# Performance work log

Measured on AMD Instinct MI355X. Metric: run time of the kernel, lower is better.

The kernel has to match this reference:

```python
import jax, jax.numpy as jnp
import numpy as np

N_NODES = 50000
N_EDGES = 400000
IN_CH = 256
HID = 64
OUT_CH = 64
HEADS = 4
N_NTYPES = 3
N_ETYPES = 4
EDGE_DIM = 32
NEG_SLOPE = 0.2
LN_EPS = 1e-5


def _glorot(key, shape, fan_in, fan_out):
    gain = float(np.sqrt(2.0))  # calculate_gain('relu')
    limit = gain * np.sqrt(6.0 / (fan_in + fan_out))
    return jax.random.uniform(key, shape, jnp.float32, -limit, limit)


def setup_inputs() -> dict:
    key = jax.random.key(0)
    ks = jax.random.split(key, 24)
    HC1 = HEADS * HID
    inp = {
        'x': jax.random.normal(ks[0], (N_NODES, IN_CH), jnp.float32),
        'edge_index': jax.random.randint(ks[1], (2, N_EDGES), 0, N_NODES, jnp.int32),
        'node_type': jax.random.randint(ks[2], (N_NODES,), 0, N_NTYPES, jnp.int32),
        'edge_type': jax.random.randint(ks[3], (N_EDGES,), 0, N_ETYPES, jnp.int32),
        'edge_attr': jax.random.normal(ks[4], (N_EDGES, EDGE_DIM), jnp.float32),
        # layer 1 (in -> hid, concat=True)
        'W_src1': _glorot(ks[5], (N_NTYPES, IN_CH, HC1), IN_CH, HC1),
        'W_dst1': _glorot(ks[6], (N_NTYPES, IN_CH, HC1), IN_CH, HC1),
        'att_src1': _glorot(ks[7], (N_ETYPES, HEADS, HID), HEADS, HID),
        'att_dst1': _glorot(ks[8], (N_ETYPES, HEADS, HID), HEADS, HID),
        'W_edge1': _glorot(ks[9], (N_ETYPES, EDGE_DIM, HC1), EDGE_DIM, HC1),
        'att_edge1': _glorot(ks[10], (N_ETYPES, HEADS, HID), HEADS, HID),
        'bias1': jnp.zeros((HC1,), jnp.float32),
        'ln_gamma1': jnp.ones((HC1,), jnp.float32),
        'ln_beta1': jnp.zeros((HC1,), jnp.float32),
        # layer 2 (heads*hid -> out, concat=False)
        'W_src2': _glorot(ks[11], (N_NTYPES, HC1, HEADS * OUT_CH), HC1, HEADS * OUT_CH),
        'W_dst2': _glorot(ks[12], (N_NTYPES, HC1, HEADS * OUT_CH), HC1, HEADS * OUT_CH),
        'att_src2': _glorot(ks[13], (N_ETYPES, HEADS, OUT_CH), HEADS, OUT_CH),
        'att_dst2': _glorot(ks[14], (N_ETYPES, HEADS, OUT_CH), HEADS, OUT_CH),
        'W_edge2': _glorot(ks[15], (N_ETYPES, EDGE_DIM, HEADS * OUT_CH), EDGE_DIM, HEADS * OUT_CH),
        'att_edge2': _glorot(ks[16], (N_ETYPES, HEADS, OUT_CH), HEADS, OUT_CH),
        'bias2': jnp.zeros((OUT_CH,), jnp.float32),
    }
    return inp


def _htgat_conv(x, src, dst, node_type, edge_type, edge_attr,
                W_src, W_dst, att_src, att_dst, W_edge, att_edge, bias, concat):
    N = x.shape[0]
    T_e, H, C = att_src.shape
    # type-specific linear transforms: compute all types, select by node_type
    xs = jnp.einsum('nd,tdo->nto', x, W_src)  # [N, T_n, H*C]
    x_src = jnp.take_along_axis(xs, node_type[:, None, None], axis=1)[:, 0].reshape(N, H, C)
    xd = jnp.einsum('nd,tdo->nto', x, W_dst)
    x_dst = jnp.take_along_axis(xd, node_type[:, None, None], axis=1)[:, 0].reshape(N, H, C)
    # per-(node, edge_type) attention scores, gathered per edge
    s_src = jnp.einsum('nhc,thc->nth', x_src, att_src)  # [N, T_e, H]
    s_dst = jnp.einsum('nhc,thc->nth', x_dst, att_dst)
    et = edge_type[:, None, None]
    alpha = (jnp.take_along_axis(s_src[src], et, axis=1)[:, 0]
             + jnp.take_along_axis(s_dst[dst], et, axis=1)[:, 0])  # [E, H]
    # temporal edge contribution: (edge_attr @ W_edge[t]) . att_edge[t]
    v = jnp.einsum('tdhc,thc->tdh', W_edge.reshape(T_e, -1, H, C), att_edge)
    s_edge = jnp.einsum('ed,tdh->eth', edge_attr, v)  # [E, T_e, H]
    alpha = alpha + jnp.take_along_axis(s_edge, et, axis=1)[:, 0]
    alpha = jnp.where(alpha >= 0, alpha, NEG_SLOPE * alpha)  # leaky_relu
    # segment softmax over destination nodes
    amax = jax.ops.segment_max(alpha, dst, num_segments=N)  # [N, H]
    amax = jnp.where(jnp.isfinite(amax), amax, 0.0)
    ae = jnp.exp(alpha - amax[dst])
    denom = jax.ops.segment_sum(ae, dst, num_segments=N)
    attn = ae / (denom[dst] + 1e-16)  # [E, H]
    # weighted message aggregation (dropout is identity in eval mode)
    msg = x_src[src] * attn[:, :, None]  # [E, H, C]
    out = jax.ops.segment_sum(msg, dst, num_segments=N)  # [N, H, C]
    if concat:
        return out.reshape(N, H * C) + bias
    return out.mean(axis=1) + bias


def _layer_norm(x, gamma, beta):
    mu = x.mean(axis=-1, keepdims=True)
    var = ((x - mu) ** 2).mean(axis=-1, keepdims=True)
    return (x - mu) * jax.lax.rsqrt(var + LN_EPS) * gamma + beta


def reference(x, edge_index, node_type, edge_type, edge_attr,
              W_src1, W_dst1, att_src1, att_dst1, W_edge1, att_edge1, bias1,
              ln_gamma1, ln_beta1,
              W_src2, W_dst2, att_src2, att_dst2, W_edge2, att_edge2, bias2):
    src, dst = edge_index[0], edge_index[1]
    h = _htgat_conv(x, src, dst, node_type, edge_type, edge_attr,
                    W_src1, W_dst1, att_src1, att_dst1, W_edge1, att_edge1, bias1,
                    concat=True)
    h = _layer_norm(h, ln_gamma1, ln_beta1)
    h = jax.nn.elu(h)
    out = _htgat_conv(h, src, dst, node_type, edge_type, edge_attr,
                      W_src2, W_dst2, att_src2, att_dst2, W_edge2, att_edge2, bias2,
                      concat=False)
    return out
```

## Files before the change

kernel.cpp:

```cpp
#include <hip/hip_runtime.h>

#define NN 50000
#define NE 400000
#define NH 4
#define NTY 3
#define ETY 4
#define EDIM 32
#define NBLK 196
#define BM 32
#define GGRID ((NN + BM - 1) / BM + NTY)

typedef __attribute__((ext_vector_type(8))) short bf16x8;
typedef __attribute__((ext_vector_type(4))) float f32x4;

static __device__ __forceinline__ unsigned short f2bf(float f) {
    unsigned u = __float_as_uint(f);
    unsigned r = (u + 0x7FFFu + ((u >> 16) & 1u)) >> 16;
    return (unsigned short)r;
}
static __device__ __forceinline__ float bf2f(unsigned short s) {
    return __uint_as_float(((unsigned)s) << 16);
}

__global__ __launch_bounds__(256) void prep_fold(
    const float* __restrict__ W_dst1, const float* __restrict__ att_dst1,
    const float* __restrict__ W_edge1, const float* __restrict__ att_edge1,
    const float* __restrict__ W_dst2, const float* __restrict__ att_dst2,
    const float* __restrict__ W_edge2, const float* __restrict__ att_edge2,
    ushort* __restrict__ uf1, ushort* __restrict__ uf2,
    float* __restrict__ v1, float* __restrict__ v2)
{
    int idx = blockIdx.x * 256 + threadIdx.x;
    if (idx < 24576) {
        const float* W; const float* A; ushort* U; int i;
        if (idx < 12288) { W = W_dst1; A = att_dst1; U = uf1; i = idx; }
        else             { W = W_dst2; A = att_dst2; U = uf2; i = idx - 12288; }
        int d = i & 255, h = (i >> 8) & 3, t = (i >> 10) & 3, tn = i >> 12;
        const float* wp = W + tn * 65536 + d * 256 + h * 64;
        const float* ap = A + t * 256 + h * 64;
        float s = 0.f;
        #pragma unroll 8
        for (int c = 0; c < 64; ++c) s += wp[c] * ap[c];
        int th = t * 4 + h;
        int ks = d >> 5, g = (d >> 3) & 3, e = d & 7;
        U[(size_t)tn * 4096 + ks * 512 + (g * 16 + th) * 8 + e] = f2bf(s);
    } else {
        int i = idx - 24576;
        const float* W; const float* A; float* V;
        if (i < 512) { W = W_edge1; A = att_edge1; V = v1; }
        else         { W = W_edge2; A = att_edge2; V = v2; i -= 512; }
        int d = i & 31, h = (i >> 5) & 3, t = i >> 7;
        const float* wp = W + t * (EDIM * 256) + d * 256 + h * 64;
        const float* ap = A + t * 256 + h * 64;
        float s = 0.f;
        #pragma unroll 8
        for (int c = 0; c < 64; ++c) s += wp[c] * ap[c];
        V[(t * 4 + h) * 32 + d] = s;
    }
}

__global__ __launch_bounds__(256) void prep_wt(
    const float* __restrict__ W1, const float* __restrict__ W2,
    ushort* __restrict__ Wf1, ushort* __restrict__ Wf2)
{
    int idx = blockIdx.x * 256 + threadIdx.x;
    const int HALF = 196608;
    const float* W = (idx < HALF) ? W1 : W2;
    ushort* O = (idx < HALF) ? Wf1 : Wf2;
    int i = (idx < HALF) ? idx : idx - HALF;
    int n = i & 255, k = (i >> 8) & 255, t = i >> 16;
    int c16 = n >> 4, r16 = n & 15;
    int ks = k >> 5, g = (k >> 3) & 3, e = k & 7;
    O[(size_t)t * 65536 + (c16 * 8 + ks) * 512 + (g * 16 + r16) * 8 + e] =
        f2bf(W[(size_t)t * 65536 + k * 256 + n]);
}

__global__ void hist_k(const int* __restrict__ dst, int* __restrict__ cnt)
{
    int i = blockIdx.x * 256 + threadIdx.x;
    if (i < NE) atomicAdd(&cnt[dst[i]], 1);
}

__global__ __launch_bounds__(256) void csr_blocksum(
    const int* __restrict__ cnt, const int* __restrict__ ntype,
    int* __restrict__ blks)
{
    int tid = threadIdx.x, b = blockIdx.x;
    int j = b * 256 + tid;
    int c = (j < NN) ? cnt[j] : 0;
    int t = (j < NN) ? ntype[j] : 3;
    int p = (t < 3) ? (1 << (t * 10)) : 0;
    #pragma unroll
    for (int d = 1; d < 64; d <<= 1) { c += __shfl_xor(c, d); p += __shfl_xor(p, d); }
    __shared__ int ws[2][4];
    int lane = tid & 63, w = tid >> 6;
    if (lane == 0) { ws[0][w] = c; ws[1][w] = p; }
    __syncthreads();
    if (tid == 0) {
        int C = ws[0][0] + ws[0][1] + ws[0][2] + ws[0][3];
        int P = ws[1][0] + ws[1][1] + ws[1][2] + ws[1][3];
        blks[b]            = C;
        blks[NBLK + b]     = P & 1023;
        blks[2 * NBLK + b] = (P >> 10) & 1023;
        blks[3 * NBLK + b] = (P >> 20) & 1023;
    }
}

__global__ __launch_bounds__(256) void csr_scanmid(int* __restrict__ blks,
                                                   int* __restrict__ ntoff,
                                                   int* __restrict__ gblk)
{
    __shared__ int4 part[256];
    int tid = threadIdx.x;
    int4 v = make_int4(0, 0, 0, 0);
    if (tid < NBLK)
        v = make_int4(blks[tid], blks[NBLK + tid], blks[2 * NBLK + tid], blks[3 * NBLK + tid]);
    int4 orig = v;
    part[tid] = v;
    __syncthreads();
    for (int off = 1; off < 256; off <<= 1) {
        int4 u = (tid >= off) ? part[tid - off] : make_int4(0, 0, 0, 0);
        __syncthreads();
        part[tid].x += u.x; part[tid].y += u.y; part[tid].z += u.z; part[tid].w += u.w;
        __syncthreads();
    }
    int4 inc = part[tid];
    if (tid < NBLK) {
        blks[tid]            = inc.x - orig.x;
        blks[NBLK + tid]     = inc.y - orig.y;
        blks[2 * NBLK + tid] = inc.z - orig.z;
        blks[3 * NBLK + tid] = inc.w - orig.w;
    }
    if (tid == 255) {
        ntoff[0] = 0; ntoff[1] = inc.y; ntoff[2] = inc.y + inc.z;
        ntoff[3] = inc.y + inc.z + inc.w;
        int b0 = (inc.y + BM - 1) / BM;
        int b1 = (inc.z + BM - 1) / BM;
        int b2 = (inc.w + BM - 1) / BM;
        gblk[0] = 0; gblk[1] = b0; gblk[2] = b0 + b1; gblk[3] = b0 + b1 + b2;
    }
}

__global__ __launch_bounds__(256) void csr_apply(
    const int* __restrict__ cnt, const int* __restrict__ ntype,
    const int* __restrict__ blks, const int* __restrict__ ntoff,
    int* __restrict__ row_ptr, int* __restrict__ node_perm)
{
    int tid = threadIdx.x, b = blockIdx.x;
    int j = b * 256 + tid;
    int c = (j < NN) ? cnt[j] : 0;
    int t = (j < NN) ? ntype[j] : 3;
    int p = (t < 3) ? (1 << (t * 10)) : 0;
    int lane = tid & 63, w = tid >> 6;
    int ic = c, ip = p;
    #pragma unroll
    for (int d = 1; d < 64; d <<= 1) {
        int uc = __shfl_up(ic, d), up = __shfl_up(ip, d);
        if (lane >= d) { ic += uc; ip += up; }
    }
    __shared__ int ws[2][4];
    if (lane == 63) { ws[0][w] = ic; ws[1][w] = ip; }
    __syncthreads();
    int coff = 0, poff = 0;
    for (int i = 0; i < w; ++i) { coff += ws[0][i]; poff += ws[1][i]; }
    int exc  = ic - c + coff;
    int expp = ip - p + poff;
    if (j < NN) {
        row_ptr[j] = blks[b] + exc;
        if (t < 3) {
            int tb   = blks[(t + 1) * NBLK + b];
            int tpfx = (expp >> (t * 10)) & 1023;
            node_perm[ntoff[t] + tb + tpfx] = j;
        }
    }
    if (j == 0) row_ptr[NN] = NE;
}

__global__ void scatter_k(const int* __restrict__ src, const int* __restrict__ dst,
                          const int* __restrict__ etype,
                          const int* __restrict__ row_ptr, int* __restrict__ cursor,
                          int* __restrict__ spk, int* __restrict__ e2c)
{
    int i = blockIdx.x * 256 + threadIdx.x;
    if (i >= NE) return;
    int d = dst[i];
    int pos = row_ptr[d] + atomicAdd(&cursor[d], 1);
    spk[pos] = src[i] | (etype[i] << 16);
    e2c[i] = pos;
}

__global__ __launch_bounds__(256) void sedge_k(
    const float* __restrict__ eattr, const int* __restrict__ etype,
    const int* __restrict__ e2c,
    const float* __restrict__ v1, const float* __restrict__ v2,
    float* __restrict__ sedge1c, float* __restrict__ sedge2c)
{
    __shared__ float v1l[512], v2l[512];
    int tid = threadIdx.x;
    v1l[tid] = v1[tid]; v1l[tid + 256] = v1[tid + 256];
    v2l[tid] = v2[tid]; v2l[tid + 256] = v2[tid + 256];
    __syncthreads();

    int i = blockIdx.x * 256 + tid;
    if (i >= NE) return;
    int t = etype[i];
    int pos = e2c[i];
    float4 ea[8];
    #pragma unroll
    for (int q = 0; q < 8; ++q) ea[q] = *(const float4*)(eattr + (size_t)i * 32 + q * 4);
    float4 o1, o2;
    #pragma unroll
    for (int h = 0; h < 4; ++h) {
        const float* vp1 = v1l + (t * 4 + h) * 32;
        const float* vp2 = v2l + (t * 4 + h) * 32;
        float s1 = 0.f, s2 = 0.f;
        #pragma unroll
        for (int q = 0; q < 8; ++q) {
            float4 w1 = *(const float4*)(vp1 + q * 4);
            float4 w2 = *(const float4*)(vp2 + q * 4);
            s1 += ea[q].x * w1.x + ea[q].y * w1.y + ea[q].z * w1.z + ea[q].w * w1.w;
            s2 += ea[q].x * w2.x + ea[q].y * w2.y + ea[q].z * w2.z + ea[q].w * w2.w;
        }
        ((float*)&o1)[h] = s1;
        ((float*)&o2)[h] = s2;
    }
    *(float4*)(sedge1c + (size_t)pos * 4) = o1;
    *(float4*)(sedge2c + (size_t)pos * 4) = o2;
}

__global__ __launch_bounds__(256) void gemm3_k(
    const ushort* __restrict__ xb, const float* __restrict__ xf,
    const ushort* __restrict__ Wf, const ushort* __restrict__ Uf,
    const float* __restrict__ att_src,
    const int* __restrict__ node_perm, const int* __restrict__ ntoff,
    const int* __restrict__ gblk,
    ushort* __restrict__ xout, float* __restrict__ s_dst,
    float* __restrict__ s_src)
{
    int b = blockIdx.x;
    if (b >= gblk[3]) return;
    int t = (b >= gblk[1]) + (b >= gblk[2]);
    int row0 = ntoff[t] + (b - gblk[t]) * BM;
    int seg1 = ntoff[t + 1];

    __shared__ __align__(16) ushort Xl[BM * 256];

    int tid = threadIdx.x;
    int w = tid >> 6, l = tid & 63;
    int kb = (tid & 31) * 16;

    #pragma unroll
    for (int it = 0; it < 4; ++it) {
        int row = it * 8 + (tid >> 5);
        int rp = row0 + row;
        int gr = (rp < seg1) ? node_perm[rp] : 0;
        uint4 pv;
        if (xf) {
            const char* src = (const char*)(xf + (size_t)gr * 256) + kb * 2;
            float4 f0 = *(const float4*)(src);
            float4 f1 = *(const float4*)(src + 16);
            pv.x = (unsigned)f2bf(f0.x) | ((unsigned)f2bf(f0.y) << 16);
            pv.y = (unsigned)f2bf(f0.z) | ((unsigned)f2bf(f0.w) << 16);
            pv.z = (unsigned)f2bf(f1.x) | ((unsigned)f2bf(f1.y) << 16);
            pv.w = (unsigned)f2bf(f1.z) | ((unsigned)f2bf(f1.w) << 16);
        } else {
            pv = *(const uint4*)((const char*)(xb + (size_t)gr * 256) + kb);
        }
        *(uint4*)((char*)Xl + row * 512 + (kb ^ ((row & 7) << 4))) = pv;
    }
    __syncthreads();

    int g = l >> 4, r16 = l & 15;
    const ushort* wfb = Wf + (size_t)(t * 16 + w * 4) * 8 * 512;
    const ushort* ufb = Uf + (size_t)t * 4096;

    f32x4 acc[2][4];
    #pragma unroll
    for (int i = 0; i < 2; ++i)
        #pragma unroll
        for (int j = 0; j < 4; ++j) acc[i][j] = (f32x4){0.f, 0.f, 0.f, 0.f};
    f32x4 uacc[2] = {{0.f,0.f,0.f,0.f},{0.f,0.f,0.f,0.f}};

    bf16x8 aW[4], aU, nW[4], nU;
    #pragma unroll
    for (int cf = 0; cf < 4; ++cf)
        aW[cf] = *(const bf16x8*)(wfb + (cf * 8 + 0) * 512 + l * 8);
    aU = *(const bf16x8*)(ufb + 0 * 512 + l * 8);

    #pragma unroll
    for (int ks = 0; ks < 8; ++ks) {
        if (ks < 7) {
            #pragma unroll
            for (int cf = 0; cf < 4; ++cf)
                nW[cf] = *(const bf16x8*)(wfb + (cf * 8 + ks + 1) * 512 + l * 8);
            nU = *(const bf16x8*)(ufb + (ks + 1) * 512 + l * 8);
        }
        int kbyte = ks * 64 + g * 16;
        bf16x8 b0 = *(const bf16x8*)((const char*)Xl + r16 * 512 + (kbyte ^ ((r16 & 7) << 4)));
        bf16x8 b1 = *(const bf16x8*)((const char*)Xl + (16 + r16) * 512 + (kbyte ^ (((16 + r16) & 7) << 4)));
        #pragma unroll
        for (int cf = 0; cf < 4; ++cf) {
            acc[0][cf] = __builtin_amdgcn_mfma_f32_16x16x32_bf16(aW[cf], b0, acc[0][cf], 0, 0, 0);
            acc[1][cf] = __builtin_amdgcn_mfma_f32_16x16x32_bf16(aW[cf], b1, acc[1][cf], 0, 0, 0);
        }
        uacc[0] = __builtin_amdgcn_mfma_f32_16x16x32_bf16(aU, b0, uacc[0], 0, 0, 0);
        uacc[1] = __builtin_amdgcn_mfma_f32_16x16x32_bf16(aU, b1, uacc[1], 0, 0, 0);
        if (ks < 7) {
            #pragma unroll
            for (int cf = 0; cf < 4; ++cf) aW[cf] = nW[cf];
            aU = nU;
        }
    }

    float p[4][2];
    #pragma unroll
    for (int te = 0; te < 4; ++te) { p[te][0] = 0.f; p[te][1] = 0.f; }
    #pragma unroll
    for (int te = 0; te < 4; ++te) {
        #pragma unroll
        for (int cf = 0; cf < 4; ++cf) {
            float4 av = *(const float4*)(att_src + te * 256 + w * 64 + cf * 16 + g * 4);
            #pragma unroll
            for (int fr = 0; fr < 2; ++fr) {
                p[te][fr] += acc[fr][cf][0] * av.x + acc[fr][cf][1] * av.y
                           + acc[fr][cf][2] * av.z + acc[fr][cf][3] * av.w;
            }
        }
    }
    #pragma unroll
    for (int te = 0; te < 4; ++te)
        #pragma unroll
        for (int fr = 0; fr < 2; ++fr) {
            p[te][fr] += __shfl_xor(p[te][fr], 16);
            p[te][fr] += __shfl_xor(p[te][fr], 32);
        }

    int col0 = w * 64;
    #pragma unroll
    for (int fr = 0; fr < 2; ++fr) {
        int rp = row0 + fr * 16 + r16;
        if (rp < seg1) {
            int gr = node_perm[rp];
            ushort* orow = xout + (size_t)gr * 256;
            #pragma unroll
            for (int cf = 0; cf < 4; ++cf) {
                ushort4 o;
                o.x = f2bf(acc[fr][cf][0]); o.y = f2bf(acc[fr][cf][1]);
                o.z = f2bf(acc[fr][cf][2]); o.w = f2bf(acc[fr][cf][3]);
                *(ushort4*)(orow + col0 + cf * 16 + g * 4) = o;
            }
            if (w == 0) {
                *(float4*)(s_dst + (size_t)gr * 16 + g * 4) =
                    make_float4(uacc[fr][0], uacc[fr][1], uacc[fr][2], uacc[fr][3]);
            }
            if (g == 0) {
                #pragma unroll
                for (int te = 0; te < 4; ++te)
                    s_src[(size_t)gr * 16 + te * 4 + w] = p[te][fr];
            }
        }
    }
}

static __device__ __forceinline__ float4 alpha_slot(
    int k, int n, const int* __restrict__ spk, const float* __restrict__ s_src,
    const float* __restrict__ s_dst, const float* __restrict__ sedgec, int* sOut)
{
    int pk = spk[k];
    int s = pk & 0xFFFF;
    int t = pk >> 16;
    float4 ss = *(const float4*)(s_src + (size_t)s * 16 + t * 4);
    float4 sd = *(const float4*)(s_dst + (size_t)n * 16 + t * 4);
    float4 se = *(const float4*)(sedgec + (size_t)k * 4);
    float4 a;
    a.x = ss.x + sd.x + se.x; a.x = (a.x >= 0.f) ? a.x : 0.2f * a.x;
    a.y = ss.y + sd.y + se.y; a.y = (a.y >= 0.f) ? a.y : 0.2f * a.y;
    a.z = ss.z + sd.z + se.z; a.z = (a.z >= 0.f) ? a.z : 0.2f * a.z;
    a.w = ss.w + sd.w + se.w; a.w = (a.w >= 0.f) ? a.w : 0.2f * a.w;
    *sOut = s;
    return a;
}

__global__ __launch_bounds__(256) void attn_k(
    const ushort* __restrict__ xsb, const float* __restrict__ s_src,
    const float* __restrict__ s_dst, const float* __restrict__ sedgec,
    const int* __restrict__ row_ptr, const int* __restrict__ spk,
    const float* __restrict__ bias, const float* __restrict__ gamma,
    const float* __restrict__ beta, void* __restrict__ out, int mode)
{
    __shared__ float  wlds[16][256];
    __shared__ int    slds[16][64];
    __shared__ float4 mxl[16], invl[16];

    int w = threadIdx.x >> 6;
    int lane = threadIdx.x & 63;
    int j = lane >> 4, li = lane & 15;
    int nid = w * 4 + j;
    int n = blockIdx.x * 16 + nid;
    int beg = row_ptr[n], end = row_ptr[n + 1];
    int deg = end - beg;

    int k0 = beg + li;
    bool act = li < deg;
    int sF = 0;
    float4 aF = make_float4(-1e30f, -1e30f, -1e30f, -1e30f);
    if (act) aF = alpha_slot(k0, n, spk, s_src, s_dst, sedgec, &sF);

    float4 mx = aF;
    for (int k = k0 + 16; k < end; k += 16) {
        int s2; float4 t = alpha_slot(k, n, spk, s_src, s_dst, sedgec, &s2);
        mx.x = fmaxf(mx.x, t.x); mx.y = fmaxf(mx.y, t.y);
        mx.z = fmaxf(mx.z, t.z); mx.w = fmaxf(mx.w, t.w);
    }
    #pragma unroll
    for (int d = 1; d < 16; d <<= 1) {
        mx.x = fmaxf(mx.x, __shfl_xor(mx.x, d, 16));
        mx.y = fmaxf(mx.y, __shfl_xor(mx.y, d, 16));
        mx.z = fmaxf(mx.z, __shfl_xor(mx.z, d, 16));
        mx.w = fmaxf(mx.w, __shfl_xor(mx.w, d, 16));
    }
    float4 ex = make_float4(0.f, 0.f, 0.f, 0.f);
    if (act) {
        ex.x = __expf(aF.x - mx.x); ex.y = __expf(aF.y - mx.y);
        ex.z = __expf(aF.z - mx.z); ex.w = __expf(aF.w - mx.w);
    }
    float4 sm = ex;
    for (int k = k0 + 16; k < end; k += 16) {
        int s2; float4 t = alpha_slot(k, n, spk, s_src, s_dst, sedgec, &s2);
        sm.x += __expf(t.x - mx.x); sm.y += __expf(t.y - mx.y);
        sm.z += __expf(t.z - mx.z); sm.w += __expf(t.w - mx.w);
    }
    #pragma unroll
    for (int d = 1; d < 16; d <<= 1) {
        sm.x += __shfl_xor(sm.x, d, 16); sm.y += __shfl_xor(sm.y, d, 16);
        sm.z += __shfl_xor(sm.z, d, 16); sm.w += __shfl_xor(sm.w, d, 16);
    }
    float4 inv;
    inv.x = 1.f / (sm.x + 1e-16f); inv.y = 1.f / (sm.y + 1e-16f);
    inv.z = 1.f / (sm.z + 1e-16f); inv.w = 1.f / (sm.w + 1e-16f);

    if (act) {
        *(float4*)&wlds[nid][li * 4] = make_float4(ex.x * inv.x, ex.y * inv.y,
                                                   ex.z * inv.z, ex.w * inv.w);
        slds[nid][li] = sF;
    }
    for (int k = k0 + 16; k < end && (k - beg) < 64; k += 16) {
        int s2; float4 t = alpha_slot(k, n, spk, s_src, s_dst, sedgec, &s2);
        int slot = k - beg;
        *(float4*)&wlds[nid][slot * 4] = make_float4(
            __expf(t.x - mx.x) * inv.x, __expf(t.y - mx.y) * inv.y,
            __expf(t.z - mx.z) * inv.z, __expf(t.w - mx.w) * inv.w);
        slds[nid][slot] = s2;
    }
    if (li == 0) { mxl[nid] = mx; invl[nid] = inv; }

    int h2 = lane >> 4;
    for (int jj = 0; jj < 4; ++jj) {
        int nb = w * 4 + jj;
        int nn = blockIdx.x * 16 + nb;
        int begj = __shfl(beg, jj * 16);
        int degj = __shfl(deg, jj * 16);

        float4 acc = make_float4(0.f, 0.f, 0.f, 0.f);
        int nfast = (degj < 64) ? degj : 64;
        for (int i = 0; i < nfast; ++i) {
            float wv = wlds[nb][i * 4 + h2];
            int s = slds[nb][i];
            ushort4 xv = *(const ushort4*)(xsb + (size_t)s * 256 + lane * 4);
            acc.x += wv * bf2f(xv.x);
            acc.y += wv * bf2f(xv.y);
            acc.z += wv * bf2f(xv.z);
            acc.w += wv * bf2f(xv.w);
        }
        if (degj > 64) {
            float4 mxj = mxl[nb], invj = invl[nb];
            float mxh  = (h2 == 0) ? mxj.x  : (h2 == 1) ? mxj.y  : (h2 == 2) ? mxj.z  : mxj.w;
            float invh = (h2 == 0) ? invj.x : (h2 == 1) ? invj.y : (h2 == 2) ? invj.z : invj.w;
            for (int k = begj + 64; k < begj + degj; ++k) {
                int pk = spk[k];
                int s = pk & 0xFFFF, t = pk >> 16;
                float a = s_src[(size_t)s * 16 + t * 4 + h2]
                        + s_dst[(size_t)nn * 16 + t * 4 + h2]
                        + sedgec[(size_t)k * 4 + h2];
                a = (a >= 0.f) ? a : 0.2f * a;
                float wv = __expf(a - mxh) * invh;
                ushort4 xv = *(const ushort4*)(xsb + (size_t)s * 256 + lane * 4);
                acc.x += wv * bf2f(xv.x);
                acc.y += wv * bf2f(xv.y);
                acc.z += wv * bf2f(xv.z);
                acc.w += wv * bf2f(xv.w);
            }
        }

        if (mode == 1) {
            float4 bb = *(const float4*)(bias + lane * 4);
            float vals[4] = { acc.x + bb.x, acc.y + bb.y, acc.z + bb.z, acc.w + bb.w };
            float s = vals[0] + vals[1] + vals[2] + vals[3];
            s += __shfl_xor(s, 1); s += __shfl_xor(s, 2); s += __shfl_xor(s, 4);
            s += __shfl_xor(s, 8); s += __shfl_xor(s, 16); s += __shfl_xor(s, 32);
            float mu = s * (1.f / 256.f);
            float q = 0.f;
            #pragma unroll
            for (int jq = 0; jq < 4; ++jq) { float d = vals[jq] - mu; q += d * d; }
            q += __shfl_xor(q, 1); q += __shfl_xor(q, 2); q += __shfl_xor(q, 4);
            q += __shfl_xor(q, 8); q += __shfl_xor(q, 16); q += __shfl_xor(q, 32);
            float r = rsqrtf(q * (1.f / 256.f) + 1e-5f);
            float4 gg = *(const float4*)(gamma + lane * 4);
            float4 be = *(const float4*)(beta + lane * 4);
            ushort4 o; float y;
            y = (vals[0] - mu) * r * gg.x + be.x; o.x = f2bf((y > 0.f) ? y : (__expf(y) - 1.f));
            y = (vals[1] - mu) * r * gg.y + be.y; o.y = f2bf((y > 0.f) ? y : (__expf(y) - 1.f));
            y = (vals[2] - mu) * r * gg.z + be.z; o.z = f2bf((y > 0.f) ? y : (__expf(y) - 1.f));
            y = (vals[3] - mu) * r * gg.w + be.w; o.w = f2bf((y > 0.f) ? y : (__expf(y) - 1.f));
            *(ushort4*)((ushort*)out + (size_t)nn * 256 + lane * 4) = o;
        } else {
            float4 am = acc;
            am.x += __shfl_xor(am.x, 16); am.x += __shfl_xor(am.x, 32);
            am.y += __shfl_xor(am.y, 16); am.y += __shfl_xor(am.y, 32);
            am.z += __shfl_xor(am.z, 16); am.z += __shfl_xor(am.z, 32);
            am.w += __shfl_xor(am.w, 16); am.w += __shfl_xor(am.w, 32);
            if (lane < 16) {
                float4 bb = *(const float4*)(bias + lane * 4);
                float4 o;
                o.x = am.x * 0.25f + bb.x;
                o.y = am.y * 0.25f + bb.y;
                o.z = am.z * 0.25f + bb.z;
                o.w = am.w * 0.25f + bb.w;
                *(float4*)((float*)out + (size_t)nn * 64 + lane * 4) = o;
            }
        }
    }
}

extern "C" void kernel_launch(void* const* d_in, const int* in_sizes, int n_in,
                              void* d_out, int out_size, void* d_ws, size_t ws_size,
                              hipStream_t stream)
{
    (void)in_sizes; (void)n_in; (void)out_size;
    const float* x        = (const float*)d_in[0];
    const int*   ei       = (const int*)d_in[1];
    const int*   ntype    = (const int*)d_in[2];
    const int*   etype    = (const int*)d_in[3];
    const float* eattr    = (const float*)d_in[4];
    const float* W_src1   = (const float*)d_in[5];
    const float* W_dst1   = (const float*)d_in[6];
    const float* att_src1 = (const float*)d_in[7];
    const float* att_dst1 = (const float*)d_in[8];
    const float* W_edge1  = (const float*)d_in[9];
    const float* att_edge1= (const float*)d_in[10];
    const float* bias1    = (const float*)d_in[11];
    const float* gamma1   = (const float*)d_in[12];
    const float* beta1    = (const float*)d_in[13];
    const float* W_src2   = (const float*)d_in[14];
    const float* W_dst2   = (const float*)d_in[15];
    const float* att_src2 = (const float*)d_in[16];
    const float* att_dst2 = (const float*)d_in[17];
    const float* W_edge2  = (const float*)d_in[18];
    const float* att_edge2= (const float*)d_in[19];
    const float* bias2    = (const float*)d_in[20];

    char* w = (char*)d_ws;
    size_t off = 0;
    auto carve = [&](size_t bytes) -> char* {
        char* p = w + off;
        off = (off + bytes + 255) & ~(size_t)255;
        return p;
    };
    ushort* x_srcb  = (ushort*)carve((size_t)NN * 256 * 2);
    ushort* hb      = (ushort*)carve((size_t)NN * 256 * 2);
    float* s_src    = (float*)carve((size_t)NN * 16 * 4);
    float* s_dst    = (float*)carve((size_t)NN * 16 * 4);
    float* sedge1c  = (float*)carve((size_t)NE * 4 * 4);
    float* sedge2c  = (float*)carve((size_t)NE * 4 * 4);
    int*   cnt      = (int*)carve((size_t)(2 * NN) * 4);
    int*   cursor   = cnt + NN;
    int*   row_ptr  = (int*)carve((size_t)(NN + 1) * 4);
    int*   spk      = (int*)carve((size_t)NE * 4);
    int*   e2c      = (int*)carve((size_t)NE * 4);
    int*   node_perm= (int*)carve((size_t)NN * 4);
    int*   ntoff    = (int*)carve(4 * 4);
    int*   gblk     = (int*)carve(4 * 4);
    int*   blks     = (int*)carve((size_t)(4 * NBLK) * 4);
    ushort* uf1     = (ushort*)carve(12288 * 2);
    ushort* uf2     = (ushort*)carve(12288 * 2);
    float* v1       = (float*)carve(512 * 4);
    float* v2       = (float*)carve(512 * 4);
    ushort* Wf1     = (ushort*)carve((size_t)196608 * 2);
    ushort* Wf2     = (ushort*)carve((size_t)196608 * 2);
    if (off > ws_size) return;

    const int* srca = ei;
    const int* dsta = ei + NE;

    hipMemsetAsync(cnt, 0, (size_t)(2 * NN) * 4, stream);

    prep_fold<<<100, 256, 0, stream>>>(W_dst1, att_dst1, W_edge1, att_edge1,
                                       W_dst2, att_dst2, W_edge2, att_edge2,
                                       uf1, uf2, v1, v2);
    prep_wt<<<1536, 256, 0, stream>>>(W_src1, W_src2, Wf1, Wf2);
    hist_k<<<(NE + 255) / 256, 256, 0, stream>>>(dsta, cnt);
    csr_blocksum<<<NBLK, 256, 0, stream>>>(cnt, ntype, blks);
    csr_scanmid<<<1, 256, 0, stream>>>(blks, ntoff, gblk);
    csr_apply<<<NBLK, 256, 0, stream>>>(cnt, ntype, blks, ntoff, row_ptr, node_perm);
    scatter_k<<<(NE + 255) / 256, 256, 0, stream>>>(srca, dsta, etype, row_ptr,
                                                    cursor, spk, e2c);
    sedge_k<<<(NE + 255) / 256, 256, 0, stream>>>(eattr, etype, e2c, v1, v2,
                                                  sedge1c, sedge2c);

    gemm3_k<<<GGRID, 256, 0, stream>>>(nullptr, x, Wf1, uf1, att_src1,
                                       node_perm, ntoff, gblk, x_srcb, s_dst, s_src);
    attn_k<<<NN / 16, 256, 0, stream>>>(x_srcb, s_src, s_dst, sedge1c, row_ptr, spk,
                                        bias1, gamma1, beta1, hb, 1);

    gemm3_k<<<GGRID, 256, 0, stream>>>(hb, nullptr, Wf2, uf2, att_src2,
                                       node_perm, ntoff, gblk, x_srcb, s_dst, s_src);
    attn_k<<<NN / 16, 256, 0, stream>>>(x_srcb, s_src, s_dst, sedge2c, row_ptr, spk,
                                        bias2, nullptr, nullptr, d_out, 2);
}
```

Baseline: 242.9 us.

## Store source features in type-sorted order and unroll attention gather by eight

Adds an inverse node permutation so the per-node source projections, source scores and the hidden activations are kept in type-sorted position order. The GEMM then reads and writes rows contiguously instead of through node_perm indirection, and edge source indices are remapped once at CSR build time. The attention gather loop is also padded to multiples of eight with zero-weight slots and unrolled so that more loads are in flight at once. The cost is an extra inverse-permutation array, padded dummy loads of row 0, and scattered writes of the layer-1 output.

```diff
diff --git a/kernel.cpp b/kernel.cpp
--- a/kernel.cpp
+++ b/kernel.cpp
@@ -144,7 +144,8 @@
 __global__ __launch_bounds__(256) void csr_apply(
     const int* __restrict__ cnt, const int* __restrict__ ntype,
     const int* __restrict__ blks, const int* __restrict__ ntoff,
-    int* __restrict__ row_ptr, int* __restrict__ node_perm)
+    int* __restrict__ row_ptr, int* __restrict__ node_perm,
+    int* __restrict__ inv_perm)
 {
     int tid = threadIdx.x, b = blockIdx.x;
     int j = b * 256 + tid;
@@ -170,14 +171,16 @@
         if (t < 3) {
             int tb   = blks[(t + 1) * NBLK + b];
             int tpfx = (expp >> (t * 10)) & 1023;
-            node_perm[ntoff[t] + tb + tpfx] = j;
+            int pos  = ntoff[t] + tb + tpfx;
+            node_perm[pos] = j;
+            inv_perm[j] = pos;
         }
     }
     if (j == 0) row_ptr[NN] = NE;
 }
 
 __global__ void scatter_k(const int* __restrict__ src, const int* __restrict__ dst,
-                          const int* __restrict__ etype,
+                          const int* __restrict__ etype, const int* __restrict__ inv,
                           const int* __restrict__ row_ptr, int* __restrict__ cursor,
                           int* __restrict__ spk, int* __restrict__ e2c)
 {
@@ -185,7 +188,7 @@
     if (i >= NE) return;
     int d = dst[i];
     int pos = row_ptr[d] + atomicAdd(&cursor[d], 1);
-    spk[pos] = src[i] | (etype[i] << 16);
+    spk[pos] = inv[src[i]] | (etype[i] << 16);
     e2c[i] = pos;
 }
 
@@ -253,9 +256,10 @@
     for (int it = 0; it < 4; ++it) {
         int row = it * 8 + (tid >> 5);
         int rp = row0 + row;
-        int gr = (rp < seg1) ? node_perm[rp] : 0;
+        int rr = (rp < seg1) ? rp : seg1 - 1;
         uint4 pv;
         if (xf) {
+            int gr = node_perm[rr];
             const char* src = (const char*)(xf + (size_t)gr * 256) + kb * 2;
             float4 f0 = *(const float4*)(src);
             float4 f1 = *(const float4*)(src + 16);
@@ -264,7 +268,7 @@
             pv.z = (unsigned)f2bf(f1.x) | ((unsigned)f2bf(f1.y) << 16);
             pv.w = (unsigned)f2bf(f1.z) | ((unsigned)f2bf(f1.w) << 16);
         } else {
-            pv = *(const uint4*)((const char*)(xb + (size_t)gr * 256) + kb);
+            pv = *(const uint4*)((const char*)(xb + (size_t)rr * 256) + kb);
         }
         *(uint4*)((char*)Xl + row * 512 + (kb ^ ((row & 7) << 4))) = pv;
     }
@@ -340,8 +344,7 @@
     for (int fr = 0; fr < 2; ++fr) {
         int rp = row0 + fr * 16 + r16;
         if (rp < seg1) {
-            int gr = node_perm[rp];
-            ushort* orow = xout + (size_t)gr * 256;
+            ushort* orow = xout + (size_t)rp * 256;
             #pragma unroll
             for (int cf = 0; cf < 4; ++cf) {
                 ushort4 o;
@@ -350,13 +353,14 @@
                 *(ushort4*)(orow + col0 + cf * 16 + g * 4) = o;
             }
             if (w == 0) {
+                int gr = node_perm[rp];
                 *(float4*)(s_dst + (size_t)gr * 16 + g * 4) =
                     make_float4(uacc[fr][0], uacc[fr][1], uacc[fr][2], uacc[fr][3]);
             }
             if (g == 0) {
                 #pragma unroll
                 for (int te = 0; te < 4; ++te)
-                    s_src[(size_t)gr * 16 + te * 4 + w] = p[te][fr];
+                    s_src[(size_t)rp * 16 + te * 4 + w] = p[te][fr];
             }
         }
     }
@@ -385,6 +389,7 @@
     const ushort* __restrict__ xsb, const float* __restrict__ s_src,
     const float* __restrict__ s_dst, const float* __restrict__ sedgec,
     const int* __restrict__ row_ptr, const int* __restrict__ spk,
+    const int* __restrict__ inv,
     const float* __restrict__ bias, const float* __restrict__ gamma,
     const float* __restrict__ beta, void* __restrict__ out, int mode)
 {
@@ -435,24 +440,32 @@
         sm.x += __shfl_xor(sm.x, d, 16); sm.y += __shfl_xor(sm.y, d, 16);
         sm.z += __shfl_xor(sm.z, d, 16); sm.w += __shfl_xor(sm.w, d, 16);
     }
-    float4 inv;
-    inv.x = 1.f / (sm.x + 1e-16f); inv.y = 1.f / (sm.y + 1e-16f);
-    inv.z = 1.f / (sm.z + 1e-16f); inv.w = 1.f / (sm.w + 1e-16f);
+    float4 inv4;
+    inv4.x = 1.f / (sm.x + 1e-16f); inv4.y = 1.f / (sm.y + 1e-16f);
+    inv4.z = 1.f / (sm.z + 1e-16f); inv4.w = 1.f / (sm.w + 1e-16f);
 
     if (act) {
-        *(float4*)&wlds[nid][li * 4] = make_float4(ex.x * inv.x, ex.y * inv.y,
-                                                   ex.z * inv.z, ex.w * inv.w);
+        *(float4*)&wlds[nid][li * 4] = make_float4(ex.x * inv4.x, ex.y * inv4.y,
+                                                   ex.z * inv4.z, ex.w * inv4.w);
         slds[nid][li] = sF;
     }
     for (int k = k0 + 16; k < end && (k - beg) < 64; k += 16) {
         int s2; float4 t = alpha_slot(k, n, spk, s_src, s_dst, sedgec, &s2);
         int slot = k - beg;
         *(float4*)&wlds[nid][slot * 4] = make_float4(
-            __expf(t.x - mx.x) * inv.x, __expf(t.y - mx.y) * inv.y,
-            __expf(t.z - mx.z) * inv.z, __expf(t.w - mx.w) * inv.w);
+            __expf(t.x - mx.x) * inv4.x, __expf(t.y - mx.y) * inv4.y,
+            __expf(t.z - mx.z) * inv4.z, __expf(t.w - mx.w) * inv4.w);
         slds[nid][slot] = s2;
     }
-    if (li == 0) { mxl[nid] = mx; invl[nid] = inv; }
+    {
+        int nf = (deg < 64) ? deg : 64;
+        int pad = ((nf + 7) & ~7) - nf;
+        if (li < pad) {
+            *(float4*)&wlds[nid][(nf + li) * 4] = make_float4(0.f, 0.f, 0.f, 0.f);
+            slds[nid][nf + li] = 0;
+        }
+    }
+    if (li == 0) { mxl[nid] = mx; invl[nid] = inv4; }
 
     int h2 = lane >> 4;
     for (int jj = 0; jj < 4; ++jj) {
@@ -463,14 +476,18 @@
 
         float4 acc = make_float4(0.f, 0.f, 0.f, 0.f);
         int nfast = (degj < 64) ? degj : 64;
-        for (int i = 0; i < nfast; ++i) {
-            float wv = wlds[nb][i * 4 + h2];
-            int s = slds[nb][i];
-            ushort4 xv = *(const ushort4*)(xsb + (size_t)s * 256 + lane * 4);
-            acc.x += wv * bf2f(xv.x);
-            acc.y += wv * bf2f(xv.y);
-            acc.z += wv * bf2f(xv.z);
-            acc.w += wv * bf2f(xv.w);
+        int nR = (nfast + 7) & ~7;
+        for (int i = 0; i < nR; i += 8) {
+            #pragma unroll
+            for (int u = 0; u < 8; ++u) {
+                float wv = wlds[nb][(i + u) * 4 + h2];
+                int s = slds[nb][i + u];
+                ushort4 xv = *(const ushort4*)(xsb + (size_t)s * 256 + lane * 4);
+                acc.x += wv * bf2f(xv.x);
+                acc.y += wv * bf2f(xv.y);
+                acc.z += wv * bf2f(xv.z);
+                acc.w += wv * bf2f(xv.w);
+            }
         }
         if (degj > 64) {
             float4 mxj = mxl[nb], invj = invl[nb];
@@ -512,7 +529,8 @@
             y = (vals[1] - mu) * r * gg.y + be.y; o.y = f2bf((y > 0.f) ? y : (__expf(y) - 1.f));
             y = (vals[2] - mu) * r * gg.z + be.z; o.z = f2bf((y > 0.f) ? y : (__expf(y) - 1.f));
             y = (vals[3] - mu) * r * gg.w + be.w; o.w = f2bf((y > 0.f) ? y : (__expf(y) - 1.f));
-            *(ushort4*)((ushort*)out + (size_t)nn * 256 + lane * 4) = o;
+            int npos = inv[nn];
+            *(ushort4*)((ushort*)out + (size_t)npos * 256 + lane * 4) = o;
         } else {
             float4 am = acc;
             am.x += __shfl_xor(am.x, 16); am.x += __shfl_xor(am.x, 32);
@@ -578,6 +596,7 @@
     int*   spk      = (int*)carve((size_t)NE * 4);
     int*   e2c      = (int*)carve((size_t)NE * 4);
     int*   node_perm= (int*)carve((size_t)NN * 4);
+    int*   inv_perm = (int*)carve((size_t)NN * 4);
     int*   ntoff    = (int*)carve(4 * 4);
     int*   gblk     = (int*)carve(4 * 4);
     int*   blks     = (int*)carve((size_t)(4 * NBLK) * 4);
@@ -601,19 +620,20 @@
     hist_k<<<(NE + 255) / 256, 256, 0, stream>>>(dsta, cnt);
     csr_blocksum<<<NBLK, 256, 0, stream>>>(cnt, ntype, blks);
     csr_scanmid<<<1, 256, 0, stream>>>(blks, ntoff, gblk);
-    csr_apply<<<NBLK, 256, 0, stream>>>(cnt, ntype, blks, ntoff, row_ptr, node_perm);
-    scatter_k<<<(NE + 255) / 256, 256, 0, stream>>>(srca, dsta, etype, row_ptr,
-                                                    cursor, spk, e2c);
+    csr_apply<<<NBLK, 256, 0, stream>>>(cnt, ntype, blks, ntoff, row_ptr,
+                                        node_perm, inv_perm);
+    scatter_k<<<(NE + 255) / 256, 256, 0, stream>>>(srca, dsta, etype, inv_perm,
+                                                    row_ptr, cursor, spk, e2c);
     sedge_k<<<(NE + 255) / 256, 256, 0, stream>>>(eattr, etype, e2c, v1, v2,
                                                   sedge1c, sedge2c);
 
     gemm3_k<<<GGRID, 256, 0, stream>>>(nullptr, x, Wf1, uf1, att_src1,
                                        node_perm, ntoff, gblk, x_srcb, s_dst, s_src);
     attn_k<<<NN / 16, 256, 0, stream>>>(x_srcb, s_src, s_dst, sedge1c, row_ptr, spk,
-                                        bias1, gamma1, beta1, hb, 1);
+                                        inv_perm, bias1, gamma1, beta1, hb, 1);
 
     gemm3_k<<<GGRID, 256, 0, stream>>>(hb, nullptr, Wf2, uf2, att_src2,
                                        node_perm, ntoff, gblk, x_srcb, s_dst, s_src);
     attn_k<<<NN / 16, 256, 0, stream>>>(x_srcb, s_src, s_dst, sedge2c, row_ptr, spk,
-                                        bias2, nullptr, nullptr, d_out, 2);
-}
+                                        inv_perm, bias2, nullptr, nullptr, d_out, 2);
+}
```

Measured after the change: 232.8 us, median of 2. 1.04x faster.
